# Kernel tuning notes

Measured on AMD Instinct MI355X. Metric: run time of the kernel, lower is better.

Reference implementation:

```python
import jax, jax.numpy as jnp
import numpy as np

B, H, KVH, HD, S = 16, 32, 8, 128, 4096
D = H * HD  # 4096
Q = 1  # decode: one query token per batch element


def rotate_half(x):
    half = x.shape[-1] // 2
    return jnp.concatenate([-x[..., half:], x[..., :half]], axis=-1)


def setup_inputs() -> dict:
    key = jax.random.key(0)
    ks = jax.random.split(key, 8)
    hidden_states = jax.random.normal(ks[0], (B, Q, D), dtype=jnp.float32)
    current_steps = jax.random.randint(ks[1], (B,), 0, S - 1)
    # additive causal mask per batch: positions <= current_step visible
    pos = jnp.arange(S)[None, :]
    attention_mask = jnp.where(pos <= current_steps[:, None], 0.0, -1e9).astype(jnp.float32)[:, None, None, :]  # [B,1,1,S]
    # RoPE cos/sin at each batch element's current position
    inv_freq = 1.0 / (10000.0 ** (jnp.arange(0, HD, 2, dtype=jnp.float32) / HD))
    ang = current_steps[:, None].astype(jnp.float32) * inv_freq[None, :]  # [B, HD/2]
    ang = jnp.concatenate([ang, ang], axis=-1)  # [B, HD]
    cos = jnp.cos(ang)[:, None, None, :]  # [B,1,1,HD]
    sin = jnp.sin(ang)[:, None, None, :]
    past_key = jax.random.normal(ks[2], (B, KVH, S, HD), dtype=jnp.float32)
    past_value = jax.random.normal(ks[3], (B, KVH, S, HD), dtype=jnp.float32)
    sc = 1.0 / np.sqrt(D)
    Wq = jax.random.normal(ks[4], (D, H * HD), dtype=jnp.float32) * sc
    Wk = jax.random.normal(ks[5], (D, KVH * HD), dtype=jnp.float32) * sc
    Wv = jax.random.normal(ks[6], (D, KVH * HD), dtype=jnp.float32) * sc
    Wo = jax.random.normal(ks[7], (H * HD, D), dtype=jnp.float32) * sc
    return dict(hidden_states=hidden_states, attention_mask=attention_mask,
                current_steps=current_steps, cos=cos, sin=sin,
                past_key=past_key, past_value=past_value,
                Wq=Wq, Wk=Wk, Wv=Wv, Wo=Wo)


def reference(hidden_states, attention_mask, current_steps, cos, sin,
              past_key, past_value, Wq, Wk, Wv, Wo):
    b, q_len, d = hidden_states.shape
    # projections -> [B, heads, Q, HD]
    q = (hidden_states @ Wq).reshape(b, q_len, H, HD).transpose(0, 2, 1, 3)
    k = (hidden_states @ Wk).reshape(b, q_len, KVH, HD).transpose(0, 2, 1, 3)
    v = (hidden_states @ Wv).reshape(b, q_len, KVH, HD).transpose(0, 2, 1, 3)
    # RoPE
    q = q * cos + rotate_half(q) * sin
    k = k * cos + rotate_half(k) * sin
    # KV-cache scatter at current_step per batch (slice_scatter equivalent)
    def upd(cache_b, new_b, step):
        return jax.lax.dynamic_update_slice(cache_b, new_b, (0, step, 0))
    new_key = jax.vmap(upd)(past_key, k, current_steps)      # [B,KVH,S,HD]
    new_value = jax.vmap(upd)(past_value, v, current_steps)  # [B,KVH,S,HD]
    # GQA attention
    g = H // KVH
    qg = q.reshape(b, KVH, g, q_len, HD)
    scores = jnp.einsum('bkgqd,bksd->bkgqs', qg, new_key) / np.sqrt(HD)
    scores = scores + attention_mask[:, :, None, :, :]  # [B,1,1,Q,S] broadcast
    probs = jax.nn.softmax(scores, axis=-1)
    out = jnp.einsum('bkgqs,bksd->bkgqd', probs, new_value)
    out = out.reshape(b, H, q_len, HD).transpose(0, 2, 1, 3).reshape(b, q_len, H * HD)
    attn_out = out @ Wo
    return attn_out, new_key, new_value
```

## Files before the change

### kernel.cpp

```cpp
#include <hip/hip_runtime.h>

#define B 16
#define H 32
#define KVH 8
#define HD 128
#define S 4096
#define D 4096
#define NQKV 6144
#define PSPLIT 32
#define WSPLIT 32
#define NCH 16
#define CROWS (S / NCH)
#define SCALE 0.08838834764831845f

typedef float nfloat4 __attribute__((ext_vector_type(4)));

__device__ __forceinline__ float4 ntload4(const float4* p) {
  nfloat4 r = __builtin_nontemporal_load(reinterpret_cast<const nfloat4*>(p));
  return *reinterpret_cast<float4*>(&r);
}
__device__ __forceinline__ void ntstore4(float4* p, float4 v) {
  __builtin_nontemporal_store(*reinterpret_cast<nfloat4*>(&v),
                              reinterpret_cast<nfloat4*>(p));
}

__global__ void k_proj(const float* __restrict__ hs, const float* __restrict__ Wq,
                       const float* __restrict__ Wk, const float* __restrict__ Wv,
                       float* __restrict__ part) {
  int n = blockIdx.x * 256 + threadIdx.x;
  int k0 = blockIdx.y * (D / PSPLIT);
  const float* w; int ldw, col;
  if (n < 4096)      { w = Wq; ldw = 4096; col = n; }
  else if (n < 5120) { w = Wk; ldw = 1024; col = n - 4096; }
  else               { w = Wv; ldw = 1024; col = n - 5120; }
  float acc[B];
#pragma unroll
  for (int b = 0; b < B; b++) acc[b] = 0.f;
  const float* wp = w + (size_t)k0 * ldw + col;
#pragma unroll 8
  for (int k = 0; k < D / PSPLIT; k++) {
    float wv = wp[(size_t)k * ldw];
#pragma unroll
    for (int b = 0; b < B; b++) acc[b] = fmaf(hs[b * D + k0 + k], wv, acc[b]);
  }
  float* p = part + (size_t)blockIdx.y * (B * NQKV);
#pragma unroll
  for (int b = 0; b < B; b++) p[(size_t)b * NQKV + n] = acc[b];
}

__global__ void k_reduce_rope(const float* __restrict__ part, const float* __restrict__ cosb,
                              const float* __restrict__ sinb, const int* __restrict__ steps,
                              float* __restrict__ qr, float* __restrict__ nkrow,
                              float* __restrict__ nvrow) {
  int i = blockIdx.x * 256 + threadIdx.x;
  int b = i / NQKV, n = i % NQKV;
  float v = 0.f;
#pragma unroll
  for (int c = 0; c < PSPLIT; c++) v += part[(size_t)c * B * NQKV + (size_t)b * NQKV + n];
  if (n < 5120) {
    int d = n & 127;
    int pn = (d < 64) ? n + 64 : n - 64;
    float pv = 0.f;
#pragma unroll
    for (int c = 0; c < PSPLIT; c++) pv += part[(size_t)c * B * NQKV + (size_t)b * NQKV + pn];
    float rot = (d < 64) ? -pv : pv;
    float r = v * cosb[b * HD + d] + rot * sinb[b * HD + d];
    if (n < 4096) qr[(size_t)b * D + n] = r;
    else          nkrow[(size_t)b * KVH * HD + (n - 4096)] = r;
  } else {
    nvrow[(size_t)b * KVH * HD + (n - 5120)] = v;
  }
}

__global__ void k_fusedK(const float* __restrict__ pastk, const float* __restrict__ nkrow,
                         const float* __restrict__ qr, const int* __restrict__ steps,
                         float* __restrict__ newk, float* __restrict__ scores) {
  int ch = blockIdx.x, kvh = blockIdx.y, b = blockIdx.z;
  int t = threadIdx.x;
  int ln = t & 15, rg = t >> 4;
  __shared__ float sbuf[CROWS][4];
  int s0 = ch * CROWS;
  int step = steps[b];
  int L = step + 1;
  int h0 = kvh * 4;
  const float4* qbase = (const float4*)(qr + ((size_t)b * H + h0) * HD);
  float4 q0[4], q1[4];
#pragma unroll
  for (int h = 0; h < 4; h++) {
    q0[h] = qbase[h * 32 + ln];
    q1[h] = qbase[h * 32 + ln + 16];
  }
  const float4* subp = (const float4*)(nkrow + (size_t)(b * KVH + kvh) * HD);
  float4 sub0 = subp[ln], sub1 = subp[ln + 16];
  const float4* src = (const float4*)(pastk + ((size_t)(b * KVH + kvh) * S + s0) * HD);
  float4*       dst = (float4*)(newk + ((size_t)(b * KVH + kvh) * S + s0) * HD);
#pragma unroll 4
  for (int it = 0; it < CROWS / 16; ++it) {
    int row = it * 16 + rg;
    size_t o0 = (size_t)row * 32 + ln;
    float4 k0 = ntload4(&src[o0]);
    float4 k1 = ntload4(&src[o0 + 16]);
    if (s0 + row == step) { k0 = sub0; k1 = sub1; }
    ntstore4(&dst[o0], k0);
    ntstore4(&dst[o0 + 16], k1);
    if (s0 + it * 16 < L) {
      float a0, a1, a2, a3;
      a0 = fmaf(k0.x, q0[0].x, fmaf(k0.y, q0[0].y, fmaf(k0.z, q0[0].z, fmaf(k0.w, q0[0].w,
           fmaf(k1.x, q1[0].x, fmaf(k1.y, q1[0].y, fmaf(k1.z, q1[0].z, k1.w * q1[0].w)))))));
      a1 = fmaf(k0.x, q0[1].x, fmaf(k0.y, q0[1].y, fmaf(k0.z, q0[1].z, fmaf(k0.w, q0[1].w,
           fmaf(k1.x, q1[1].x, fmaf(k1.y, q1[1].y, fmaf(k1.z, q1[1].z, k1.w * q1[1].w)))))));
      a2 = fmaf(k0.x, q0[2].x, fmaf(k0.y, q0[2].y, fmaf(k0.z, q0[2].z, fmaf(k0.w, q0[2].w,
           fmaf(k1.x, q1[2].x, fmaf(k1.y, q1[2].y, fmaf(k1.z, q1[2].z, k1.w * q1[2].w)))))));
      a3 = fmaf(k0.x, q0[3].x, fmaf(k0.y, q0[3].y, fmaf(k0.z, q0[3].z, fmaf(k0.w, q0[3].w,
           fmaf(k1.x, q1[3].x, fmaf(k1.y, q1[3].y, fmaf(k1.z, q1[3].z, k1.w * q1[3].w)))))));
#pragma unroll
      for (int o = 1; o < 16; o <<= 1) {
        a0 += __shfl_xor(a0, o);
        a1 += __shfl_xor(a1, o);
        a2 += __shfl_xor(a2, o);
        a3 += __shfl_xor(a3, o);
      }
      if (ln < 4) {
        float my = (ln == 0) ? a0 : (ln == 1) ? a1 : (ln == 2) ? a2 : a3;
        sbuf[row][ln] = my * SCALE;
      }
    }
  }
  if (s0 < L) {
    __syncthreads();
    float* srow = scores + (size_t)(b * H + h0) * S + s0;
#pragma unroll
    for (int j = 0; j < 4; ++j) srow[(size_t)j * S + t] = sbuf[t][j];
  }
}

__global__ void k_smax(float* __restrict__ scores, const int* __restrict__ steps) {
  int bid = blockIdx.x;
  int b = bid >> 5, h = bid & 31;
  int t = threadIdx.x;
  __shared__ float red[4];
  int L = steps[b] + 1;
  float* srow = scores + (size_t)(b * H + h) * S;
  float lmax = -1e30f;
  for (int s = t; s < L; s += 256) lmax = fmaxf(lmax, srow[s]);
#pragma unroll
  for (int o = 32; o > 0; o >>= 1) lmax = fmaxf(lmax, __shfl_xor(lmax, o));
  if ((t & 63) == 0) red[t >> 6] = lmax;
  __syncthreads();
  float gm = fmaxf(fmaxf(red[0], red[1]), fmaxf(red[2], red[3]));
  float lsum = 0.f;
  for (int s = t; s < L; s += 256) {
    float p = __expf(srow[s] - gm);
    srow[s] = p;
    lsum += p;
  }
#pragma unroll
  for (int o = 32; o > 0; o >>= 1) lsum += __shfl_xor(lsum, o);
  __syncthreads();
  if ((t & 63) == 0) red[t >> 6] = lsum;
  __syncthreads();
  float inv = 1.f / (red[0] + red[1] + red[2] + red[3]);
  for (int s = t; s < L; s += 256) srow[s] *= inv;
}

__global__ void k_fusedV(const float* __restrict__ pastv, const float* __restrict__ nvrow,
                         const float* __restrict__ probs, const int* __restrict__ steps,
                         float* __restrict__ newv, float* __restrict__ part) {
  int ch = blockIdx.x, kvh = blockIdx.y, b = blockIdx.z;
  int t = threadIdx.x;
  int d4 = t & 31, rr = t >> 5;
  __shared__ float pbuf[CROWS][4];
  int s0 = ch * CROWS;
  int step = steps[b];
  int L = step + 1;
  int h0 = kvh * 4;
  bool any = (s0 < L);
  float4 subv = ((const float4*)(nvrow + (size_t)(b * KVH + kvh) * HD))[d4];
  const float4* src = (const float4*)(pastv + ((size_t)(b * KVH + kvh) * S + s0) * HD);
  float4*       dst = (float4*)(newv + ((size_t)(b * KVH + kvh) * S + s0) * HD);
  if (any) {
    const float* pb = probs + (size_t)(b * H + h0) * S + s0;
#pragma unroll
    for (int j = 0; j < 4; ++j)
      pbuf[t][j] = (s0 + t < L) ? pb[(size_t)j * S + t] : 0.f;
    __syncthreads();
  }
  float4 a0 = make_float4(0.f, 0.f, 0.f, 0.f), a1 = a0, a2 = a0, a3 = a0;
#pragma unroll 4
  for (int i = 0; i < CROWS / 8; ++i) {
    int r = i * 8 + rr;
    float4 v = ntload4(&src[r * 32 + d4]);
    if (s0 + r == step) v = subv;
    ntstore4(&dst[r * 32 + d4], v);
    if (any && i * 8 < L - s0) {
      float q0 = pbuf[r][0], q1 = pbuf[r][1], q2 = pbuf[r][2], q3 = pbuf[r][3];
      a0.x = fmaf(q0, v.x, a0.x); a0.y = fmaf(q0, v.y, a0.y);
      a0.z = fmaf(q0, v.z, a0.z); a0.w = fmaf(q0, v.w, a0.w);
      a1.x = fmaf(q1, v.x, a1.x); a1.y = fmaf(q1, v.y, a1.y);
      a1.z = fmaf(q1, v.z, a1.z); a1.w = fmaf(q1, v.w, a1.w);
      a2.x = fmaf(q2, v.x, a2.x); a2.y = fmaf(q2, v.y, a2.y);
      a2.z = fmaf(q2, v.z, a2.z); a2.w = fmaf(q2, v.w, a2.w);
      a3.x = fmaf(q3, v.x, a3.x); a3.y = fmaf(q3, v.y, a3.y);
      a3.z = fmaf(q3, v.z, a3.z); a3.w = fmaf(q3, v.w, a3.w);
    }
  }
  a0.x += __shfl_xor(a0.x, 32); a0.y += __shfl_xor(a0.y, 32);
  a0.z += __shfl_xor(a0.z, 32); a0.w += __shfl_xor(a0.w, 32);
  a1.x += __shfl_xor(a1.x, 32); a1.y += __shfl_xor(a1.y, 32);
  a1.z += __shfl_xor(a1.z, 32); a1.w += __shfl_xor(a1.w, 32);
  a2.x += __shfl_xor(a2.x, 32); a2.y += __shfl_xor(a2.y, 32);
  a2.z += __shfl_xor(a2.z, 32); a2.w += __shfl_xor(a2.w, 32);
  a3.x += __shfl_xor(a3.x, 32); a3.y += __shfl_xor(a3.y, 32);
  a3.z += __shfl_xor(a3.z, 32); a3.w += __shfl_xor(a3.w, 32);
  __shared__ float4 red[4][4][32];
  int w = t >> 6;
  __syncthreads();
  if ((t & 32) == 0) {
    red[w][0][d4] = a0; red[w][1][d4] = a1; red[w][2][d4] = a2; red[w][3][d4] = a3;
  }
  __syncthreads();
  if (t < 128) {
    int hh = t >> 5, dd = t & 31;
    float4 x0 = red[0][hh][dd], x1 = red[1][hh][dd], x2 = red[2][hh][dd], x3 = red[3][hh][dd];
    float4 s;
    s.x = (x0.x + x1.x) + (x2.x + x3.x);
    s.y = (x0.y + x1.y) + (x2.y + x3.y);
    s.z = (x0.z + x1.z) + (x2.z + x3.z);
    s.w = (x0.w + x1.w) + (x2.w + x3.w);
    ((float4*)(part + (((size_t)ch * B + b) * KVH + kvh) * 512))[t] = s;
  }
}

__global__ void k_reduce_ctx(const float* __restrict__ part, float* __restrict__ ctx) {
  int i = blockIdx.x * 256 + threadIdx.x;
  int b = i >> 12, r = i & 4095, h = r >> 7, d = r & 127;
  int kvh = h >> 2, hl = h & 3;
  float s = 0.f;
#pragma unroll
  for (int c = 0; c < NCH; c++)
    s += part[(((size_t)c * B + b) * KVH + kvh) * 512 + hl * 128 + d];
  ctx[i] = s;
}

__global__ void k_wo(const float* __restrict__ ctx, const float* __restrict__ Wo,
                     float* __restrict__ part) {
  int n = blockIdx.x * 256 + threadIdx.x;
  int k0 = blockIdx.y * (D / WSPLIT);
  float acc[B];
#pragma unroll
  for (int b = 0; b < B; b++) acc[b] = 0.f;
  const float* wp = Wo + (size_t)k0 * D + n;
#pragma unroll 8
  for (int k = 0; k < D / WSPLIT; k++) {
    float wv = wp[(size_t)k * D];
#pragma unroll
    for (int b = 0; b < B; b++) acc[b] = fmaf(ctx[b * D + k0 + k], wv, acc[b]);
  }
  float* p = part + (size_t)blockIdx.y * (B * D);
#pragma unroll
  for (int b = 0; b < B; b++) p[(size_t)b * D + n] = acc[b];
}

__global__ void k_reduce_out(const float* __restrict__ part, float* __restrict__ out) {
  int i = blockIdx.x * 256 + threadIdx.x;
  float s = 0.f;
#pragma unroll
  for (int c = 0; c < WSPLIT; c++) s += part[(size_t)c * B * D + i];
  out[i] = s;
}

extern "C" void kernel_launch(void* const* d_in, const int* in_sizes, int n_in,
                              void* d_out, int out_size, void* d_ws, size_t ws_size,
                              hipStream_t stream) {
  const float* hs    = (const float*)d_in[0];
  const int*   steps = (const int*)d_in[2];
  const float* cosb  = (const float*)d_in[3];
  const float* sinb  = (const float*)d_in[4];
  const float* pk    = (const float*)d_in[5];
  const float* pvv   = (const float*)d_in[6];
  const float* Wq    = (const float*)d_in[7];
  const float* Wk    = (const float*)d_in[8];
  const float* Wv    = (const float*)d_in[9];
  const float* Wo    = (const float*)d_in[10];

  float* attn_out = (float*)d_out;
  float* newk = attn_out + (size_t)B * D;
  float* newv = newk + (size_t)B * KVH * S * HD;

  float* ws = (float*)d_ws;
  float* A        = ws;
  float* p_part   = A;
  float* p_scores = A;
  float* p_wopart = A;
  float* p_pvpart = A + 3145728;
  float* p_qr     = p_pvpart + 1048576;
  float* p_nkrow  = p_qr + (size_t)B * D;
  float* p_nvrow  = p_nkrow + (size_t)B * KVH * HD;
  float* p_ctx    = p_nvrow + (size_t)B * KVH * HD;

  hipLaunchKernelGGL(k_proj, dim3(NQKV / 256, PSPLIT), dim3(256), 0, stream,
                     hs, Wq, Wk, Wv, p_part);
  hipLaunchKernelGGL(k_reduce_rope, dim3(B * NQKV / 256), dim3(256), 0, stream,
                     p_part, cosb, sinb, steps, p_qr, p_nkrow, p_nvrow);
  hipLaunchKernelGGL(k_fusedK, dim3(NCH, KVH, B), dim3(256), 0, stream,
                     pk, p_nkrow, p_qr, steps, newk, p_scores);
  hipLaunchKernelGGL(k_smax, dim3(B * H), dim3(256), 0, stream,
                     p_scores, steps);
  hipLaunchKernelGGL(k_fusedV, dim3(NCH, KVH, B), dim3(256), 0, stream,
                     pvv, p_nvrow, p_scores, steps, newv, p_pvpart);
  hipLaunchKernelGGL(k_reduce_ctx, dim3(B * D / 256), dim3(256), 0, stream,
                     p_pvpart, p_ctx);
  hipLaunchKernelGGL(k_wo, dim3(D / 256, WSPLIT), dim3(256), 0, stream,
                     p_ctx, Wo, p_wopart);
  hipLaunchKernelGGL(k_reduce_out, dim3(B * D / 256), dim3(256), 0, stream,
                     p_wopart, attn_out);
}
```

Baseline: 316.9 us.

## Fuse K scoring, softmax and V accumulation into one split-KV flash kernel

Merges the separate K-copy/score kernel, the softmax kernel and the V-copy/accumulate kernel into one kernel. Each chunk computes a local max and sum-of-exponentials, and a final reduction rescales and combines the chunks (flash-decoding style). This removes the global scores round trip and two kernel launches. Each block now streams both K and V, so it runs longer and uses more registers and shared memory. The RoPE reduce is also reworked so one thread handles a lo/hi pair, which avoids reading the partial sums twice.

```diff
diff --git a/kernel.cpp b/kernel.cpp
--- a/kernel.cpp
+++ b/kernel.cpp
@@ -53,155 +53,166 @@
                               float* __restrict__ qr, float* __restrict__ nkrow,
                               float* __restrict__ nvrow) {
   int i = blockIdx.x * 256 + threadIdx.x;
-  int b = i / NQKV, n = i % NQKV;
-  float v = 0.f;
-#pragma unroll
-  for (int c = 0; c < PSPLIT; c++) v += part[(size_t)c * B * NQKV + (size_t)b * NQKV + n];
-  if (n < 5120) {
-    int d = n & 127;
-    int pn = (d < 64) ? n + 64 : n - 64;
-    float pv = 0.f;
-#pragma unroll
-    for (int c = 0; c < PSPLIT; c++) pv += part[(size_t)c * B * NQKV + (size_t)b * NQKV + pn];
-    float rot = (d < 64) ? -pv : pv;
-    float r = v * cosb[b * HD + d] + rot * sinb[b * HD + d];
-    if (n < 4096) qr[(size_t)b * D + n] = r;
-    else          nkrow[(size_t)b * KVH * HD + (n - 4096)] = r;
+  int b = i / 3584, n2 = i % 3584;
+  if (n2 < 2560) {
+    int hr = n2 >> 6, d = n2 & 63;
+    int n_lo = hr * 128 + d, n_hi = n_lo + 64;
+    float vlo = 0.f, vhi = 0.f;
+#pragma unroll
+    for (int c = 0; c < PSPLIT; c++) {
+      const float* pc = part + (size_t)c * B * NQKV + (size_t)b * NQKV;
+      vlo += pc[n_lo];
+      vhi += pc[n_hi];
+    }
+    float clo = cosb[b * HD + d], chi = cosb[b * HD + d + 64];
+    float slo = sinb[b * HD + d], shi = sinb[b * HD + d + 64];
+    float rlo = vlo * clo - vhi * slo;
+    float rhi = vhi * chi + vlo * shi;
+    if (n_lo < 4096) {
+      qr[(size_t)b * D + n_lo] = rlo;
+      qr[(size_t)b * D + n_hi] = rhi;
+    } else {
+      nkrow[(size_t)b * KVH * HD + (n_lo - 4096)] = rlo;
+      nkrow[(size_t)b * KVH * HD + (n_hi - 4096)] = rhi;
+    }
   } else {
-    nvrow[(size_t)b * KVH * HD + (n - 5120)] = v;
-  }
-}
-
-__global__ void k_fusedK(const float* __restrict__ pastk, const float* __restrict__ nkrow,
-                         const float* __restrict__ qr, const int* __restrict__ steps,
-                         float* __restrict__ newk, float* __restrict__ scores) {
+    int j = n2 - 2560;
+    float v = 0.f;
+#pragma unroll
+    for (int c = 0; c < PSPLIT; c++)
+      v += part[(size_t)c * B * NQKV + (size_t)b * NQKV + 5120 + j];
+    nvrow[(size_t)b * KVH * HD + j] = v;
+  }
+}
+
+__global__ void k_flashKV(const float* __restrict__ pastk, const float* __restrict__ pastv,
+                          const float* __restrict__ nkrow, const float* __restrict__ nvrow,
+                          const float* __restrict__ qr, const int* __restrict__ steps,
+                          float* __restrict__ newk, float* __restrict__ newv,
+                          float* __restrict__ part, float* __restrict__ stats) {
   int ch = blockIdx.x, kvh = blockIdx.y, b = blockIdx.z;
   int t = threadIdx.x;
-  int ln = t & 15, rg = t >> 4;
   __shared__ float sbuf[CROWS][4];
-  int s0 = ch * CROWS;
-  int step = steps[b];
-  int L = step + 1;
-  int h0 = kvh * 4;
-  const float4* qbase = (const float4*)(qr + ((size_t)b * H + h0) * HD);
-  float4 q0[4], q1[4];
-#pragma unroll
-  for (int h = 0; h < 4; h++) {
-    q0[h] = qbase[h * 32 + ln];
-    q1[h] = qbase[h * 32 + ln + 16];
-  }
-  const float4* subp = (const float4*)(nkrow + (size_t)(b * KVH + kvh) * HD);
-  float4 sub0 = subp[ln], sub1 = subp[ln + 16];
-  const float4* src = (const float4*)(pastk + ((size_t)(b * KVH + kvh) * S + s0) * HD);
-  float4*       dst = (float4*)(newk + ((size_t)(b * KVH + kvh) * S + s0) * HD);
-#pragma unroll 4
-  for (int it = 0; it < CROWS / 16; ++it) {
-    int row = it * 16 + rg;
-    size_t o0 = (size_t)row * 32 + ln;
-    float4 k0 = ntload4(&src[o0]);
-    float4 k1 = ntload4(&src[o0 + 16]);
-    if (s0 + row == step) { k0 = sub0; k1 = sub1; }
-    ntstore4(&dst[o0], k0);
-    ntstore4(&dst[o0 + 16], k1);
-    if (s0 + it * 16 < L) {
-      float a0, a1, a2, a3;
-      a0 = fmaf(k0.x, q0[0].x, fmaf(k0.y, q0[0].y, fmaf(k0.z, q0[0].z, fmaf(k0.w, q0[0].w,
-           fmaf(k1.x, q1[0].x, fmaf(k1.y, q1[0].y, fmaf(k1.z, q1[0].z, k1.w * q1[0].w)))))));
-      a1 = fmaf(k0.x, q0[1].x, fmaf(k0.y, q0[1].y, fmaf(k0.z, q0[1].z, fmaf(k0.w, q0[1].w,
-           fmaf(k1.x, q1[1].x, fmaf(k1.y, q1[1].y, fmaf(k1.z, q1[1].z, k1.w * q1[1].w)))))));
-      a2 = fmaf(k0.x, q0[2].x, fmaf(k0.y, q0[2].y, fmaf(k0.z, q0[2].z, fmaf(k0.w, q0[2].w,
-           fmaf(k1.x, q1[2].x, fmaf(k1.y, q1[2].y, fmaf(k1.z, q1[2].z, k1.w * q1[2].w)))))));
-      a3 = fmaf(k0.x, q0[3].x, fmaf(k0.y, q0[3].y, fmaf(k0.z, q0[3].z, fmaf(k0.w, q0[3].w,
-           fmaf(k1.x, q1[3].x, fmaf(k1.y, q1[3].y, fmaf(k1.z, q1[3].z, k1.w * q1[3].w)))))));
-#pragma unroll
-      for (int o = 1; o < 16; o <<= 1) {
-        a0 += __shfl_xor(a0, o);
-        a1 += __shfl_xor(a1, o);
-        a2 += __shfl_xor(a2, o);
-        a3 += __shfl_xor(a3, o);
-      }
-      if (ln < 4) {
-        float my = (ln == 0) ? a0 : (ln == 1) ? a1 : (ln == 2) ? a2 : a3;
-        sbuf[row][ln] = my * SCALE;
-      }
-    }
-  }
-  if (s0 < L) {
-    __syncthreads();
-    float* srow = scores + (size_t)(b * H + h0) * S + s0;
-#pragma unroll
-    for (int j = 0; j < 4; ++j) srow[(size_t)j * S + t] = sbuf[t][j];
-  }
-}
-
-__global__ void k_smax(float* __restrict__ scores, const int* __restrict__ steps) {
-  int bid = blockIdx.x;
-  int b = bid >> 5, h = bid & 31;
-  int t = threadIdx.x;
-  __shared__ float red[4];
-  int L = steps[b] + 1;
-  float* srow = scores + (size_t)(b * H + h) * S;
-  float lmax = -1e30f;
-  for (int s = t; s < L; s += 256) lmax = fmaxf(lmax, srow[s]);
-#pragma unroll
-  for (int o = 32; o > 0; o >>= 1) lmax = fmaxf(lmax, __shfl_xor(lmax, o));
-  if ((t & 63) == 0) red[t >> 6] = lmax;
-  __syncthreads();
-  float gm = fmaxf(fmaxf(red[0], red[1]), fmaxf(red[2], red[3]));
-  float lsum = 0.f;
-  for (int s = t; s < L; s += 256) {
-    float p = __expf(srow[s] - gm);
-    srow[s] = p;
-    lsum += p;
-  }
-#pragma unroll
-  for (int o = 32; o > 0; o >>= 1) lsum += __shfl_xor(lsum, o);
-  __syncthreads();
-  if ((t & 63) == 0) red[t >> 6] = lsum;
-  __syncthreads();
-  float inv = 1.f / (red[0] + red[1] + red[2] + red[3]);
-  for (int s = t; s < L; s += 256) srow[s] *= inv;
-}
-
-__global__ void k_fusedV(const float* __restrict__ pastv, const float* __restrict__ nvrow,
-                         const float* __restrict__ probs, const int* __restrict__ steps,
-                         float* __restrict__ newv, float* __restrict__ part) {
-  int ch = blockIdx.x, kvh = blockIdx.y, b = blockIdx.z;
-  int t = threadIdx.x;
-  int d4 = t & 31, rr = t >> 5;
-  __shared__ float pbuf[CROWS][4];
+  __shared__ float redm[4][4];
+  __shared__ float4 red4[4][4][32];
   int s0 = ch * CROWS;
   int step = steps[b];
   int L = step + 1;
   int h0 = kvh * 4;
   bool any = (s0 < L);
-  float4 subv = ((const float4*)(nvrow + (size_t)(b * KVH + kvh) * HD))[d4];
-  const float4* src = (const float4*)(pastv + ((size_t)(b * KVH + kvh) * S + s0) * HD);
-  float4*       dst = (float4*)(newv + ((size_t)(b * KVH + kvh) * S + s0) * HD);
-  if (any) {
-    const float* pb = probs + (size_t)(b * H + h0) * S + s0;
-#pragma unroll
-    for (int j = 0; j < 4; ++j)
-      pbuf[t][j] = (s0 + t < L) ? pb[(size_t)j * S + t] : 0.f;
-    __syncthreads();
-  }
+  int w = t >> 6;
+
+  {
+    int ln = t & 15, rg = t >> 4;
+    const float4* qbase = (const float4*)(qr + ((size_t)b * H + h0) * HD);
+    float4 q0[4], q1[4];
+#pragma unroll
+    for (int h = 0; h < 4; h++) {
+      q0[h] = qbase[h * 32 + ln];
+      q1[h] = qbase[h * 32 + ln + 16];
+    }
+    const float4* subp = (const float4*)(nkrow + (size_t)(b * KVH + kvh) * HD);
+    float4 sub0 = subp[ln], sub1 = subp[ln + 16];
+    const float4* src = (const float4*)(pastk + ((size_t)(b * KVH + kvh) * S + s0) * HD);
+    float4*       dst = (float4*)(newk + ((size_t)(b * KVH + kvh) * S + s0) * HD);
+#pragma unroll 4
+    for (int it = 0; it < CROWS / 16; ++it) {
+      int row = it * 16 + rg;
+      size_t o0 = (size_t)row * 32 + ln;
+      float4 k0 = ntload4(&src[o0]);
+      float4 k1 = ntload4(&src[o0 + 16]);
+      if (s0 + row == step) { k0 = sub0; k1 = sub1; }
+      ntstore4(&dst[o0], k0);
+      ntstore4(&dst[o0 + 16], k1);
+      if (s0 + it * 16 < L) {
+        float a0, a1, a2, a3;
+        a0 = fmaf(k0.x, q0[0].x, fmaf(k0.y, q0[0].y, fmaf(k0.z, q0[0].z, fmaf(k0.w, q0[0].w,
+             fmaf(k1.x, q1[0].x, fmaf(k1.y, q1[0].y, fmaf(k1.z, q1[0].z, k1.w * q1[0].w)))))));
+        a1 = fmaf(k0.x, q0[1].x, fmaf(k0.y, q0[1].y, fmaf(k0.z, q0[1].z, fmaf(k0.w, q0[1].w,
+             fmaf(k1.x, q1[1].x, fmaf(k1.y, q1[1].y, fmaf(k1.z, q1[1].z, k1.w * q1[1].w)))))));
+        a2 = fmaf(k0.x, q0[2].x, fmaf(k0.y, q0[2].y, fmaf(k0.z, q0[2].z, fmaf(k0.w, q0[2].w,
+             fmaf(k1.x, q1[2].x, fmaf(k1.y, q1[2].y, fmaf(k1.z, q1[2].z, k1.w * q1[2].w)))))));
+        a3 = fmaf(k0.x, q0[3].x, fmaf(k0.y, q0[3].y, fmaf(k0.z, q0[3].z, fmaf(k0.w, q0[3].w,
+             fmaf(k1.x, q1[3].x, fmaf(k1.y, q1[3].y, fmaf(k1.z, q1[3].z, k1.w * q1[3].w)))))));
+#pragma unroll
+        for (int o = 1; o < 16; o <<= 1) {
+          a0 += __shfl_xor(a0, o);
+          a1 += __shfl_xor(a1, o);
+          a2 += __shfl_xor(a2, o);
+          a3 += __shfl_xor(a3, o);
+        }
+        if (ln < 4) {
+          float my = (ln == 0) ? a0 : (ln == 1) ? a1 : (ln == 2) ? a2 : a3;
+          sbuf[row][ln] = my * SCALE;
+        }
+      }
+    }
+  }
+  __syncthreads();
+
+  bool valid = any && (s0 + t < L);
+  float s_0 = valid ? sbuf[t][0] : -1e30f;
+  float s_1 = valid ? sbuf[t][1] : -1e30f;
+  float s_2 = valid ? sbuf[t][2] : -1e30f;
+  float s_3 = valid ? sbuf[t][3] : -1e30f;
+  float mx0 = s_0, mx1 = s_1, mx2 = s_2, mx3 = s_3;
+#pragma unroll
+  for (int o = 1; o < 64; o <<= 1) {
+    mx0 = fmaxf(mx0, __shfl_xor(mx0, o));
+    mx1 = fmaxf(mx1, __shfl_xor(mx1, o));
+    mx2 = fmaxf(mx2, __shfl_xor(mx2, o));
+    mx3 = fmaxf(mx3, __shfl_xor(mx3, o));
+  }
+  if ((t & 63) == 0) { redm[w][0] = mx0; redm[w][1] = mx1; redm[w][2] = mx2; redm[w][3] = mx3; }
+  __syncthreads();
+  float m0 = fmaxf(fmaxf(redm[0][0], redm[1][0]), fmaxf(redm[2][0], redm[3][0]));
+  float m1 = fmaxf(fmaxf(redm[0][1], redm[1][1]), fmaxf(redm[2][1], redm[3][1]));
+  float m2 = fmaxf(fmaxf(redm[0][2], redm[1][2]), fmaxf(redm[2][2], redm[3][2]));
+  float m3 = fmaxf(fmaxf(redm[0][3], redm[1][3]), fmaxf(redm[2][3], redm[3][3]));
+  float e0 = valid ? __expf(s_0 - m0) : 0.f;
+  float e1 = valid ? __expf(s_1 - m1) : 0.f;
+  float e2 = valid ? __expf(s_2 - m2) : 0.f;
+  float e3 = valid ? __expf(s_3 - m3) : 0.f;
+  float es0 = e0, es1 = e1, es2 = e2, es3 = e3;
+#pragma unroll
+  for (int o = 1; o < 64; o <<= 1) {
+    es0 += __shfl_xor(es0, o);
+    es1 += __shfl_xor(es1, o);
+    es2 += __shfl_xor(es2, o);
+    es3 += __shfl_xor(es3, o);
+  }
+  __syncthreads();
+  if ((t & 63) == 0) { redm[w][0] = es0; redm[w][1] = es1; redm[w][2] = es2; redm[w][3] = es3; }
+  sbuf[t][0] = e0; sbuf[t][1] = e1; sbuf[t][2] = e2; sbuf[t][3] = e3;
+  __syncthreads();
+  float l0 = redm[0][0] + redm[1][0] + redm[2][0] + redm[3][0];
+  float l1 = redm[0][1] + redm[1][1] + redm[2][1] + redm[3][1];
+  float l2 = redm[0][2] + redm[1][2] + redm[2][2] + redm[3][2];
+  float l3 = redm[0][3] + redm[1][3] + redm[2][3] + redm[3][3];
+
+  int d4 = t & 31, rr = t >> 5;
   float4 a0 = make_float4(0.f, 0.f, 0.f, 0.f), a1 = a0, a2 = a0, a3 = a0;
+  {
+    float4 vsub = ((const float4*)(nvrow + (size_t)(b * KVH + kvh) * HD))[d4];
+    const float4* src = (const float4*)(pastv + ((size_t)(b * KVH + kvh) * S + s0) * HD);
+    float4*       dst = (float4*)(newv + ((size_t)(b * KVH + kvh) * S + s0) * HD);
 #pragma unroll 4
-  for (int i = 0; i < CROWS / 8; ++i) {
-    int r = i * 8 + rr;
-    float4 v = ntload4(&src[r * 32 + d4]);
-    if (s0 + r == step) v = subv;
-    ntstore4(&dst[r * 32 + d4], v);
-    if (any && i * 8 < L - s0) {
-      float q0 = pbuf[r][0], q1 = pbuf[r][1], q2 = pbuf[r][2], q3 = pbuf[r][3];
-      a0.x = fmaf(q0, v.x, a0.x); a0.y = fmaf(q0, v.y, a0.y);
-      a0.z = fmaf(q0, v.z, a0.z); a0.w = fmaf(q0, v.w, a0.w);
-      a1.x = fmaf(q1, v.x, a1.x); a1.y = fmaf(q1, v.y, a1.y);
-      a1.z = fmaf(q1, v.z, a1.z); a1.w = fmaf(q1, v.w, a1.w);
-      a2.x = fmaf(q2, v.x, a2.x); a2.y = fmaf(q2, v.y, a2.y);
-      a2.z = fmaf(q2, v.z, a2.z); a2.w = fmaf(q2, v.w, a2.w);
-      a3.x = fmaf(q3, v.x, a3.x); a3.y = fmaf(q3, v.y, a3.y);
-      a3.z = fmaf(q3, v.z, a3.z); a3.w = fmaf(q3, v.w, a3.w);
+    for (int i = 0; i < CROWS / 8; ++i) {
+      int r = i * 8 + rr;
+      float4 v = ntload4(&src[r * 32 + d4]);
+      if (s0 + r == step) v = vsub;
+      ntstore4(&dst[r * 32 + d4], v);
+      if (any && i * 8 < L - s0) {
+        float q0 = sbuf[r][0], q1 = sbuf[r][1], q2 = sbuf[r][2], q3 = sbuf[r][3];
+        a0.x = fmaf(q0, v.x, a0.x); a0.y = fmaf(q0, v.y, a0.y);
+        a0.z = fmaf(q0, v.z, a0.z); a0.w = fmaf(q0, v.w, a0.w);
+        a1.x = fmaf(q1, v.x, a1.x); a1.y = fmaf(q1, v.y, a1.y);
+        a1.z = fmaf(q1, v.z, a1.z); a1.w = fmaf(q1, v.w, a1.w);
+        a2.x = fmaf(q2, v.x, a2.x); a2.y = fmaf(q2, v.y, a2.y);
+        a2.z = fmaf(q2, v.z, a2.z); a2.w = fmaf(q2, v.w, a2.w);
+        a3.x = fmaf(q3, v.x, a3.x); a3.y = fmaf(q3, v.y, a3.y);
+        a3.z = fmaf(q3, v.z, a3.z); a3.w = fmaf(q3, v.w, a3.w);
+      }
     }
   }
   a0.x += __shfl_xor(a0.x, 32); a0.y += __shfl_xor(a0.y, 32);
@@ -212,16 +223,14 @@
   a2.z += __shfl_xor(a2.z, 32); a2.w += __shfl_xor(a2.w, 32);
   a3.x += __shfl_xor(a3.x, 32); a3.y += __shfl_xor(a3.y, 32);
   a3.z += __shfl_xor(a3.z, 32); a3.w += __shfl_xor(a3.w, 32);
-  __shared__ float4 red[4][4][32];
-  int w = t >> 6;
   __syncthreads();
   if ((t & 32) == 0) {
-    red[w][0][d4] = a0; red[w][1][d4] = a1; red[w][2][d4] = a2; red[w][3][d4] = a3;
+    red4[w][0][d4] = a0; red4[w][1][d4] = a1; red4[w][2][d4] = a2; red4[w][3][d4] = a3;
   }
   __syncthreads();
   if (t < 128) {
     int hh = t >> 5, dd = t & 31;
-    float4 x0 = red[0][hh][dd], x1 = red[1][hh][dd], x2 = red[2][hh][dd], x3 = red[3][hh][dd];
+    float4 x0 = red4[0][hh][dd], x1 = red4[1][hh][dd], x2 = red4[2][hh][dd], x3 = red4[3][hh][dd];
     float4 s;
     s.x = (x0.x + x1.x) + (x2.x + x3.x);
     s.y = (x0.y + x1.y) + (x2.y + x3.y);
@@ -229,17 +238,33 @@
     s.w = (x0.w + x1.w) + (x2.w + x3.w);
     ((float4*)(part + (((size_t)ch * B + b) * KVH + kvh) * 512))[t] = s;
   }
-}
-
-__global__ void k_reduce_ctx(const float* __restrict__ part, float* __restrict__ ctx) {
+  if (t == 0) {
+    size_t si = (((size_t)ch * B + b) * KVH + kvh) * 8;
+    stats[si + 0] = m0; stats[si + 1] = l0;
+    stats[si + 2] = m1; stats[si + 3] = l1;
+    stats[si + 4] = m2; stats[si + 5] = l2;
+    stats[si + 6] = m3; stats[si + 7] = l3;
+  }
+}
+
+__global__ void k_reduce_ctx(const float* __restrict__ part, const float* __restrict__ stats,
+                             float* __restrict__ ctx) {
   int i = blockIdx.x * 256 + threadIdx.x;
   int b = i >> 12, r = i & 4095, h = r >> 7, d = r & 127;
   int kvh = h >> 2, hl = h & 3;
-  float s = 0.f;
+  float M = -1e30f;
 #pragma unroll
   for (int c = 0; c < NCH; c++)
-    s += part[(((size_t)c * B + b) * KVH + kvh) * 512 + hl * 128 + d];
-  ctx[i] = s;
+    M = fmaxf(M, stats[(((size_t)c * B + b) * KVH + kvh) * 8 + hl * 2]);
+  float num = 0.f, den = 0.f;
+#pragma unroll
+  for (int c = 0; c < NCH; c++) {
+    size_t si = (((size_t)c * B + b) * KVH + kvh) * 8 + hl * 2;
+    float wgt = __expf(stats[si] - M);
+    den += wgt * stats[si + 1];
+    num += wgt * part[(((size_t)c * B + b) * KVH + kvh) * 512 + hl * 128 + d];
+  }
+  ctx[i] = num / den;
 }
 
 __global__ void k_wo(const float* __restrict__ ctx, const float* __restrict__ Wo,
@@ -290,26 +315,23 @@
   float* ws = (float*)d_ws;
   float* A        = ws;
   float* p_part   = A;
-  float* p_scores = A;
   float* p_wopart = A;
   float* p_pvpart = A + 3145728;
-  float* p_qr     = p_pvpart + 1048576;
+  float* p_stats  = p_pvpart + 1048576;
+  float* p_qr     = p_stats + 16384;
   float* p_nkrow  = p_qr + (size_t)B * D;
   float* p_nvrow  = p_nkrow + (size_t)B * KVH * HD;
   float* p_ctx    = p_nvrow + (size_t)B * KVH * HD;
 
   hipLaunchKernelGGL(k_proj, dim3(NQKV / 256, PSPLIT), dim3(256), 0, stream,
                      hs, Wq, Wk, Wv, p_part);
-  hipLaunchKernelGGL(k_reduce_rope, dim3(B * NQKV / 256), dim3(256), 0, stream,
+  hipLaunchKernelGGL(k_reduce_rope, dim3(B * 3584 / 256), dim3(256), 0, stream,
                      p_part, cosb, sinb, steps, p_qr, p_nkrow, p_nvrow);
-  hipLaunchKernelGGL(k_fusedK, dim3(NCH, KVH, B), dim3(256), 0, stream,
-                     pk, p_nkrow, p_qr, steps, newk, p_scores);
-  hipLaunchKernelGGL(k_smax, dim3(B * H), dim3(256), 0, stream,
-                     p_scores, steps);
-  hipLaunchKernelGGL(k_fusedV, dim3(NCH, KVH, B), dim3(256), 0, stream,
-                     pvv, p_nvrow, p_scores, steps, newv, p_pvpart);
+  hipLaunchKernelGGL(k_flashKV, dim3(NCH, KVH, B), dim3(256), 0, stream,
+                     pk, pvv, p_nkrow, p_nvrow, p_qr, steps, newk, newv,
+                     p_pvpart, p_stats);
   hipLaunchKernelGGL(k_reduce_ctx, dim3(B * D / 256), dim3(256), 0, stream,
-                     p_pvpart, p_ctx);
+                     p_pvpart, p_stats, p_ctx);
   hipLaunchKernelGGL(k_wo, dim3(D / 256, WSPLIT), dim3(256), 0, stream,
                      p_ctx, Wo, p_wopart);
   hipLaunchKernelGGL(k_reduce_out, dim3(B * D / 256), dim3(256), 0, stream,
```

Result: faster. 309.0 us (-2.5%).
